# Kernel tuning notes

Measured on AMD Instinct MI355X. Metric: run time of the kernel, lower is better.

Reference implementation:

```python
import jax, jax.numpy as jnp
import numpy as np
from jax import lax

EPS = 2e-05


def _conv2d(x, w, b, stride):
    # x: [B,C,H,W], w: [O,I,3,3] (OIHW), VALID padding
    y = lax.conv_general_dilated(x, w, (stride, stride), 'VALID',
                                 dimension_numbers=('NCHW', 'OIHW', 'NCHW'))
    return y + b[None, :, None, None]


def _reflect_pad(x):
    return jnp.pad(x, ((0, 0), (0, 0), (1, 1), (1, 1)), mode='reflect')


def _transfer(cont_feat, styl_feat):
    # cont_feat, styl_feat: [B, N, H, W]
    B, N, H, W = cont_feat.shape
    xc = cont_feat.reshape(B, N, -1)   # [B,N,Mc]
    xs = styl_feat.reshape(B, N, -1)   # [B,N,Ms]
    I = jnp.eye(N, dtype=xc.dtype)

    # whitening of content
    mc = jnp.mean(xc, axis=-1, keepdims=True)
    xc0 = xc - mc
    cov_c = jnp.einsum('bnm,bkm->bnk', xc0, xc0) / (xc0.shape[-1] - 1)
    Lc = jnp.linalg.cholesky(cov_c + EPS * I)  # eps*I regularization (torch retry loop)
    inv_Lc = jnp.linalg.inv(Lc)
    whiten = jnp.einsum('bnk,bkm->bnm', inv_Lc, xc0)

    # coloring with style statistics
    ms = jnp.mean(xs, axis=-1, keepdims=True)
    xs0 = xs - ms
    cov_s = jnp.einsum('bnm,bkm->bnk', xs0, xs0) / (xs0.shape[-1] - 1)
    Ls = jnp.linalg.cholesky(cov_s + EPS * I)
    colored = jnp.einsum('bnk,bkm->bnm', Ls, whiten) + ms
    return colored.reshape(B, N, H, W)


def setup_inputs() -> dict:
    key = jax.random.key(0)
    k1, k2, k3, k4 = jax.random.split(key, 4)
    B, C, H, W = 8, 128, 256, 256
    cont_feat = jax.random.normal(k1, (B, C, H, W), dtype=jnp.float32)
    styl_feat = jax.random.normal(k2, (B, C, H, W), dtype=jnp.float32)
    # conv params (kaiming-ish scaling)
    fan1 = C * 9
    W1 = jax.random.normal(k3, (C, C, 3, 3), dtype=jnp.float32) / np.sqrt(fan1)
    b1 = jnp.zeros((C,), dtype=jnp.float32)
    W2 = jax.random.normal(k4, (2 * C, C, 3, 3), dtype=jnp.float32) / np.sqrt(fan1)
    b2 = jnp.zeros((2 * C,), dtype=jnp.float32)
    return {'cont_feat': cont_feat, 'styl_feat': styl_feat,
            'W1': W1, 'b1': b1, 'W2': W2, 'b2': b2}


def reference(cont_feat, styl_feat, W1, b1, W2, b2):
    cs = _transfer(cont_feat, styl_feat)          # [B,C,H,W]
    x = _conv2d(_reflect_pad(cs), W1, b1, 2)      # [B,C,H/2,W/2]
    x = jax.nn.relu(x)
    out = _conv2d(_reflect_pad(x), W2, b2, 1)     # [B,2C,H/2,W/2]
    return out
```

## Files before the change

### kernel.cpp

```cpp
#include <hip/hip_runtime.h>
#include <hip/hip_bf16.h>

#define B_  8
#define C_  128
#define M_  65536
#define EPSV 2e-05f

typedef __attribute__((ext_vector_type(8))) short bf16x8;
typedef __attribute__((ext_vector_type(4))) float f32x4;

#define MFMA(a, b, c) __builtin_amdgcn_mfma_f32_16x16x32_bf16((a), (b), (c), 0, 0, 0)

__device__ __forceinline__ short f2b(float f) {
    unsigned u = __float_as_uint(f);
    u = (u + 0x7FFFu + ((u >> 16) & 1u)) >> 16;
    return (short)u;
}

__device__ __forceinline__ int swz(int px, int c) {
    return px * 256 + ((((c >> 3) ^ (px & 15)) << 4) | ((c & 7) << 1));
}

__device__ __forceinline__ int rot(int i, int k) {
    return i * 128 + ((((k >> 2) + i) & 31) << 2) + (k & 3);
}

__global__ __launch_bounds__(256) void k_prep(const float* W1, const float* W2,
                                              short* wp1, short* wp2) {
    int idx = blockIdx.x * 256 + threadIdx.x;
    if (idx < 9 * 128 * 128) {
        int c = idx & 127, o = (idx >> 7) & 127, rs = idx >> 14;
        wp1[idx] = f2b(W1[(o * 128 + c) * 9 + rs]);
    }
    idx -= 9 * 128 * 128;
    if (idx >= 0 && idx < 9 * 256 * 128) {
        int c = idx & 127, o = (idx >> 7) & 255, rs = idx >> 15;
        wp2[idx] = f2b(W2[(o * 128 + c) * 9 + rs]);
    }
}

__global__ __launch_bounds__(256, 2) void k_gram(const float* cont, const float* styl,
                                                 float* part, float* S) {
    __shared__ short ls[128 * 136];
    __shared__ float ssum[128 * 32];
    int bx = blockIdx.x;
    int chunk = bx & 31, which = (bx >> 5) & 1, b = bx >> 6;
    const float* X = (which ? styl : cont) + (size_t)b * C_ * M_ + chunk * 2048;
    int tid = threadIdx.x, lane = tid & 63, wid = tid >> 6;
    int kg = tid & 31, r0 = tid >> 5;

    float sacc[16];
    #pragma unroll
    for (int p = 0; p < 16; ++p) sacc[p] = 0.f;
    f32x4 acc[2][8];
    for (int u = 0; u < 2; ++u)
        for (int j = 0; j < 8; ++j) acc[u][j] = (f32x4){0.f, 0.f, 0.f, 0.f};

    float4 pf[16];
    #pragma unroll
    for (int p = 0; p < 16; ++p)
        pf[p] = *(const float4*)(X + (size_t)(r0 + p * 8) * M_ + kg * 4);

    for (int it = 0; it < 16; ++it) {
        #pragma unroll
        for (int p = 0; p < 16; ++p) {
            int row = r0 + p * 8;
            float4 v = pf[p];
            sacc[p] += v.x + v.y + v.z + v.w;
            union { __hip_bfloat162 h[2]; unsigned long long u; } pk;
            pk.h[0] = __float22bfloat162_rn(make_float2(v.x, v.y));
            pk.h[1] = __float22bfloat162_rn(make_float2(v.z, v.w));
            *(unsigned long long*)(ls + row * 136 + kg * 4) = pk.u;
        }
        if (it < 15) {
            int kb = (it + 1) * 128;
            #pragma unroll
            for (int p = 0; p < 16; ++p)
                pf[p] = *(const float4*)(X + (size_t)(r0 + p * 8) * M_ + kb + kg * 4);
        }
        asm volatile("s_waitcnt lgkmcnt(0)" ::: "memory");
        __builtin_amdgcn_sched_barrier(0);
        __builtin_amdgcn_s_barrier();
        for (int ks = 0; ks < 4; ++ks) {
            int co = ks * 32 + (lane >> 4) * 8;
            bf16x8 a[2], bbf[8];
            for (int u = 0; u < 2; ++u) {
                int row = (wid * 2 + u) * 16 + (lane & 15);
                a[u] = *(const bf16x8*)(ls + row * 136 + co);
            }
            for (int j = 0; j < 8; ++j) {
                int row = j * 16 + (lane & 15);
                bbf[j] = *(const bf16x8*)(ls + row * 136 + co);
            }
            for (int u = 0; u < 2; ++u)
                for (int j = 0; j < 8; ++j)
                    acc[u][j] = MFMA(a[u], bbf[j], acc[u][j]);
        }
        __builtin_amdgcn_sched_barrier(0);
        __builtin_amdgcn_s_barrier();
    }
    __syncthreads();
    for (int p = 0; p < 16; ++p) ssum[(r0 + p * 8) * 32 + kg] = sacc[p];
    __syncthreads();
    float* Sp = S + ((size_t)which * 8 + b) * 128;
    if (tid < 128) {
        float s = 0.f;
        for (int q = 0; q < 32; ++q) s += ssum[tid * 32 + q];
        atomicAdd(&Sp[tid], s);
    }
    float* Pp = part + ((size_t)((which * 8 + b) * 32 + chunk)) * 16384;
    for (int u = 0; u < 2; ++u) {
        int rowb = (wid * 2 + u) * 16 + (lane >> 4) * 4;
        for (int j = 0; j < 8; ++j) {
            int col = j * 16 + (lane & 15);
            for (int e = 0; e < 4; ++e)
                Pp[(rowb + e) * 128 + col] = acc[u][j][e];
        }
    }
}

__global__ __launch_bounds__(256) void k_gsum(const float* part, float* G) {
    int idx = blockIdx.x * 256 + threadIdx.x;
    int m = idx >> 14, e = idx & 16383;
    const float* p = part + (size_t)m * 32 * 16384 + e;
    float s = 0.f;
    #pragma unroll
    for (int c = 0; c < 32; ++c) s += p[(size_t)c * 16384];
    G[idx] = s;
}

__global__ __launch_bounds__(128) void k_chol(const float* G, const float* S,
                                              float* LcT, float* Lsg) {
    __shared__ float A[128 * 128];
    int wb = blockIdx.x;
    int i = threadIdx.x;
    const float invM = 1.f / 65536.f;
    const float invM1 = 1.f / 65535.f;
    const float* Gp = G + (size_t)wb * 16384;
    const float* Sp = S + (size_t)wb * 128;
    float mui = Sp[i] * invM;

    for (int j = 0; j <= i; ++j) {
        float muj = Sp[j] * invM;
        float cv = (Gp[i * 128 + j] - 65536.f * mui * muj) * invM1;
        if (j == i) cv += EPSV;
        A[rot(i, j)] = cv;
    }
    __syncthreads();

    #pragma unroll
    for (int bb = 0; bb < 4; ++bb) {
        const int jb0 = bb * 32, bend = jb0 + 32;
        float t[32], u[32], t0[32];
        #pragma unroll
        for (int kk = 0; kk < 32; ++kk) t0[kk] = A[rot(i, jb0 + kk)];
        #pragma unroll
        for (int jj = 0; jj < 32; ++jj) {
            const int j = jb0 + jj;
            float dot = 0.f;
            #pragma unroll
            for (int kk = 0; kk < jj; ++kk)
                dot += u[kk] * A[rot(j, jb0 + kk)];
            float raw = t0[jj] - dot;
            if (i >= j) A[rot(i, j)] = raw;
            __syncthreads();
            float pr = A[rot(j, j)];
            float piv = sqrtf(pr);
            float rpj = 1.f / piv;
            float tv = (i > j) ? raw * rpj : (i == j ? piv : 0.f);
            t[jj] = tv;
            u[jj] = tv * rpj;
        }
        #pragma unroll
        for (int kk = 0; kk < 32; ++kk) {
            int j = jb0 + kk;
            if (i >= j) A[rot(i, j)] = t[kk];
        }
        __syncthreads();
        if (bb < 3) {
            if (i >= bend) {
                int jmax = (i & ~63) + 64;
                for (int j4 = bend; j4 < jmax; j4 += 4) {
                    float* rp_ = A + i * 128 + ((((j4 >> 2) + i) & 31) << 2);
                    float4 r = *(float4*)rp_;
                    #pragma unroll
                    for (int g = 0; g < 8; ++g) {
                        int kc = (jb0 >> 2) + g;
                        float4 c0 = *(const float4*)(A + (j4 + 0) * 128 + (((kc + j4 + 0) & 31) << 2));
                        float4 c1 = *(const float4*)(A + (j4 + 1) * 128 + (((kc + j4 + 1) & 31) << 2));
                        float4 c2 = *(const float4*)(A + (j4 + 2) * 128 + (((kc + j4 + 2) & 31) << 2));
                        float4 c3 = *(const float4*)(A + (j4 + 3) * 128 + (((kc + j4 + 3) & 31) << 2));
                        float ta = t[g * 4], tb = t[g * 4 + 1], tc = t[g * 4 + 2], td = t[g * 4 + 3];
                        r.x -= ta * c0.x + tb * c0.y + tc * c0.z + td * c0.w;
                        r.y -= ta * c1.x + tb * c1.y + tc * c1.z + td * c1.w;
                        r.z -= ta * c2.x + tb * c2.y + tc * c2.z + td * c2.w;
                        r.w -= ta * c3.x + tb * c3.y + tc * c3.z + td * c3.w;
                    }
                    *(float4*)rp_ = r;
                }
            }
            __syncthreads();
        }
    }
    __syncthreads();
    if (wb < 8) {
        float* dst = LcT + (size_t)wb * 16384;
        for (int j = 0; j <= i; ++j)
            dst[j * 128 + i] = A[rot(i, j)];
    } else {
        float4* dst = (float4*)(Lsg + (size_t)(wb - 8) * 16384);
        const float4* src = (const float4*)A;
        for (int t = i; t < 4096; t += 128) dst[t] = src[t];
    }
}

__global__ __launch_bounds__(128) void k_trsm(const float* LcT, const float* Lsg,
                                              const float* S, short* Tb, float* Vv) {
    __shared__ float A[128 * 128];
    int b = blockIdx.x;
    int i = threadIdx.x;
    const float invM = 1.f / 65536.f;
    const float* Lc = LcT + (size_t)b * 16384;
    {
        const float4* src = (const float4*)(Lsg + (size_t)b * 16384);
        float4* dst = (float4*)A;
        for (int t = i; t < 4096; t += 128) dst[t] = src[t];
    }
    __syncthreads();
    float lsdia = A[rot(i, i)];
    float rdia = 1.f / Lc[i * 128 + i];
    float tii = lsdia * rdia;
    __syncthreads();
    for (int j = 0; j < 127; ++j)
        if (i > j) A[rot(j, i)] = Lc[j * 128 + i];
    A[rot(i, i)] = rdia;
    __syncthreads();

    #pragma unroll
    for (int bb = 3; bb >= 0; --bb) {
        const int jb0 = bb * 32, bend = jb0 + 32;
        float t[32], ls0[32];
        #pragma unroll
        for (int kk = 0; kk < 32; ++kk) ls0[kk] = A[rot(i, jb0 + kk)];
        #pragma unroll
        for (int jj = 31; jj >= 0; --jj) {
            const int j = jb0 + jj;
            float dot = (i < bend) ? tii * A[rot(j, i)] : 0.f;
            #pragma unroll
            for (int kk = jj + 1; kk < 32; ++kk)
                dot += t[kk] * A[rot(j, jb0 + kk)];
            float val = (ls0[jj] - dot) * A[rot(j, j)];
            t[jj] = (j < i) ? val : 0.f;
        }
        #pragma unroll
        for (int kk = 0; kk < 32; ++kk) {
            int j = jb0 + kk;
            if (j < i) A[rot(i, j)] = t[kk];
            if (j == i) t[kk] = tii;
        }
        if (jb0 > 0 && i >= jb0) {
            for (int j4 = 0; j4 < jb0; j4 += 4) {
                float* rp = A + i * 128 + ((((j4 >> 2) + i) & 31) << 2);
                float4 r = *(float4*)rp;
                #pragma unroll
                for (int g = 0; g < 8; ++g) {
                    int kc = (jb0 >> 2) + g;
                    float4 c0 = *(const float4*)(A + (j4 + 0) * 128 + (((kc + j4 + 0) & 31) << 2));
                    float4 c1 = *(const float4*)(A + (j4 + 1) * 128 + (((kc + j4 + 1) & 31) << 2));
                    float4 c2 = *(const float4*)(A + (j4 + 2) * 128 + (((kc + j4 + 2) & 31) << 2));
                    float4 c3 = *(const float4*)(A + (j4 + 3) * 128 + (((kc + j4 + 3) & 31) << 2));
                    float ta = t[g * 4], tb2 = t[g * 4 + 1], tc = t[g * 4 + 2], td = t[g * 4 + 3];
                    r.x -= ta * c0.x + tb2 * c0.y + tc * c0.z + td * c0.w;
                    r.y -= ta * c1.x + tb2 * c1.y + tc * c1.z + td * c1.w;
                    r.z -= ta * c2.x + tb2 * c2.y + tc * c2.z + td * c2.w;
                    r.w -= ta * c3.x + tb2 * c3.y + tc * c3.z + td * c3.w;
                }
                *(float4*)rp = r;
            }
        }
    }
    const float* Sc = S + (size_t)b * 128;
    const float* Ss = S + (size_t)(8 + b) * 128;
    float vdot = 0.f;
    short* Tr = Tb + (size_t)b * 16384 + i * 128;
    for (int j = 0; j < 128; ++j) {
        float t = (j < i) ? A[rot(i, j)] : (j == i ? tii : 0.f);
        Tr[j] = f2b(t);
        if (j <= i) vdot += t * (Sc[j] * invM);
    }
    Vv[b * 128 + i] = Ss[i] * invM - vdot;
}

__global__ __launch_bounds__(256) void k_transform(const float* cont, const short* Tb,
                                                   const float* Vv, short* colored) {
    __shared__ short ls[16384];
    char* lsb = (char*)ls;
    int bx = blockIdx.x;
    int b = bx >> 9, p0 = (bx & 511) << 7;
    int tid = threadIdx.x, lane = tid & 63, wid = tid >> 6;

    {
        int px = tid & 127, ch = tid >> 7;
        const float* Xp = cont + (size_t)b * C_ * M_ + p0 + px;
        for (int it = 0; it < 16; ++it) {
            int c0 = it * 8 + ch * 4;
            float x0 = Xp[(size_t)(c0 + 0) * M_];
            float x1 = Xp[(size_t)(c0 + 1) * M_];
            float x2 = Xp[(size_t)(c0 + 2) * M_];
            float x3 = Xp[(size_t)(c0 + 3) * M_];
            union { short s[4]; unsigned long long u; } pk;
            pk.s[0] = f2b(x0); pk.s[1] = f2b(x1); pk.s[2] = f2b(x2); pk.s[3] = f2b(x3);
            *(unsigned long long*)(lsb + swz(px, c0)) = pk.u;
        }
    }
    __syncthreads();
    f32x4 acc[8][2];
    for (int pg = 0; pg < 8; ++pg)
        for (int u = 0; u < 2; ++u) acc[pg][u] = (f32x4){0.f, 0.f, 0.f, 0.f};
    const short* Tbase = Tb + (size_t)b * 16384;
    for (int kc = 0; kc < 4; ++kc) {
        int co = kc * 32 + (lane >> 4) * 8;
        bf16x8 bfr[2], afr[8];
        for (int u = 0; u < 2; ++u) {
            int chn = (wid * 2 + u) * 16 + (lane & 15);
            bfr[u] = *(const bf16x8*)(Tbase + chn * 128 + co);
        }
        for (int pg = 0; pg < 8; ++pg) {
            int px = pg * 16 + (lane & 15);
            afr[pg] = *(const bf16x8*)(lsb + swz(px, co));
        }
        for (int pg = 0; pg < 8; ++pg)
            for (int u = 0; u < 2; ++u)
                acc[pg][u] = MFMA(afr[pg], bfr[u], acc[pg][u]);
    }
    __syncthreads();
    for (int u = 0; u < 2; ++u) {
        int chn = (wid * 2 + u) * 16 + (lane & 15);
        float vv = Vv[b * 128 + chn];
        for (int pg = 0; pg < 8; ++pg)
            for (int e = 0; e < 4; ++e) {
                int px = pg * 16 + (lane >> 4) * 4 + e;
                *(short*)(lsb + swz(px, chn)) = f2b(acc[pg][u][e] + vv);
            }
    }
    __syncthreads();
    short* dst = colored + ((size_t)b * M_ + p0) * 128;
    for (int it = 0; it < 8; ++it) {
        int gid = tid + it * 256;
        int px = gid >> 4, gr = gid & 15;
        bf16x8 v = *(const bf16x8*)(lsb + px * 256 + ((gr ^ (px & 15)) << 4));
        *(bf16x8*)(dst + (size_t)px * 128 + gr * 8) = v;
    }
}

__global__ __launch_bounds__(256) void k_conv1(const short* colored, const short* wp1,
                                               const float* b1, short* out1) {
    __shared__ short ls[130 * 128];
    char* lsb = (char*)ls;
    int x0 = blockIdx.x * 64, y = blockIdx.y, b = blockIdx.z;
    int tid = threadIdx.x, lane = tid & 63, wid = tid >> 6;

    f32x4 acc[4][2];
    for (int pg = 0; pg < 4; ++pg)
        for (int u = 0; u < 2; ++u) acc[pg][u] = (f32x4){0.f, 0.f, 0.f, 0.f};

    for (int r = 0; r < 3; ++r) {
        int grow = 2 * y - 1 + r;
        if (grow < 0) grow = -grow;
        __syncthreads();
        const short* src = colored + ((size_t)b * M_ + grow * 256) * 128;
        for (int it = 0; it < 9; ++it) {
            int gid = tid + it * 256;
            if (gid < 130 * 16) {
                int L = gid >> 4, gr = gid & 15;
                int gcol = 2 * x0 - 1 + L;
                if (gcol < 0) gcol = -gcol;
                else if (gcol > 255) gcol = 510 - gcol;
                bf16x8 v = *(const bf16x8*)(src + (size_t)gcol * 128 + gr * 8);
                *(bf16x8*)(lsb + L * 256 + ((gr ^ (L & 15)) << 4)) = v;
            }
        }
        __syncthreads();
        for (int s = 0; s < 3; ++s)
            for (int kc = 0; kc < 4; ++kc) {
                int co = kc * 32 + (lane >> 4) * 8;
                bf16x8 afr[4], bfr[2];
                for (int pg = 0; pg < 4; ++pg) {
                    int L = (pg * 16 + (lane & 15)) * 2 + s;
                    afr[pg] = *(const bf16x8*)(lsb + swz(L, co));
                }
                const short* wb = wp1 + (r * 3 + s) * 128 * 128;
                for (int u = 0; u < 2; ++u) {
                    int o = (wid * 2 + u) * 16 + (lane & 15);
                    bfr[u] = *(const bf16x8*)(wb + o * 128 + co);
                }
                for (int pg = 0; pg < 4; ++pg)
                    for (int u = 0; u < 2; ++u)
                        acc[pg][u] = MFMA(afr[pg], bfr[u], acc[pg][u]);
            }
    }
    __syncthreads();
    for (int u = 0; u < 2; ++u) {
        int o = (wid * 2 + u) * 16 + (lane & 15);
        float bias = b1[o];
        for (int pg = 0; pg < 4; ++pg)
            for (int e = 0; e < 4; ++e) {
                int px = pg * 16 + (lane >> 4) * 4 + e;
                float v = acc[pg][u][e] + bias;
                v = v > 0.f ? v : 0.f;
                *(short*)(lsb + swz(px, o)) = f2b(v);
            }
    }
    __syncthreads();
    short* dst = out1 + ((size_t)b * 16384 + y * 128 + x0) * 128;
    for (int it = 0; it < 4; ++it) {
        int gid = tid + it * 256;
        int px = gid >> 4, gr = gid & 15;
        bf16x8 v = *(const bf16x8*)(lsb + px * 256 + ((gr ^ (px & 15)) << 4));
        *(bf16x8*)(dst + (size_t)px * 128 + gr * 8) = v;
    }
}

__global__ __launch_bounds__(256) void k_conv2(const short* out1, const short* wp2,
                                               const float* b2, float* outp) {
    __shared__ short ls[66 * 128];
    char* lsb = (char*)ls;
    int x0 = blockIdx.x * 64, y = blockIdx.y, b = blockIdx.z;
    int tid = threadIdx.x, lane = tid & 63, wid = tid >> 6;

    f32x4 acc[4][4];
    for (int pg = 0; pg < 4; ++pg)
        for (int u = 0; u < 4; ++u) acc[pg][u] = (f32x4){0.f, 0.f, 0.f, 0.f};

    for (int r = 0; r < 3; ++r) {
        int grow = y - 1 + r;
        if (grow < 0) grow = -grow;
        else if (grow > 127) grow = 254 - grow;
        __syncthreads();
        const short* src = out1 + ((size_t)b * 16384 + grow * 128) * 128;
        for (int it = 0; it < 5; ++it) {
            int gid = tid + it * 256;
            if (gid < 66 * 16) {
                int L = gid >> 4, gr = gid & 15;
                int gcol = x0 - 1 + L;
                if (gcol < 0) gcol = -gcol;
                else if (gcol > 127) gcol = 254 - gcol;
                bf16x8 v = *(const bf16x8*)(src + (size_t)gcol * 128 + gr * 8);
                *(bf16x8*)(lsb + L * 256 + ((gr ^ (L & 15)) << 4)) = v;
            }
        }
        __syncthreads();
        for (int s = 0; s < 3; ++s)
            for (int kc = 0; kc < 4; ++kc) {
                int co = kc * 32 + (lane >> 4) * 8;
                bf16x8 afr[4], bfr[4];
                for (int pg = 0; pg < 4; ++pg) {
                    int L = pg * 16 + (lane & 15) + s;
                    afr[pg] = *(const bf16x8*)(lsb + swz(L, co));
                }
                const short* wb = wp2 + (r * 3 + s) * 256 * 128;
                for (int u = 0; u < 4; ++u) {
                    int o = (wid * 4 + u) * 16 + (lane & 15);
                    bfr[u] = *(const bf16x8*)(wb + o * 128 + co);
                }
                for (int pg = 0; pg < 4; ++pg)
                    for (int u = 0; u < 4; ++u)
                        acc[pg][u] = MFMA(afr[pg], bfr[u], acc[pg][u]);
            }
    }
    for (int u = 0; u < 4; ++u) {
        int o = (wid * 4 + u) * 16 + (lane & 15);
        float bias = b2[o];
        float* dst = outp + ((size_t)b * 256 + o) * 16384 + y * 128 + x0;
        for (int pg = 0; pg < 4; ++pg) {
            float4 v;
            v.x = acc[pg][u][0] + bias;
            v.y = acc[pg][u][1] + bias;
            v.z = acc[pg][u][2] + bias;
            v.w = acc[pg][u][3] + bias;
            *(float4*)(dst + pg * 16 + (lane >> 4) * 4) = v;
        }
    }
}

extern "C" void kernel_launch(void* const* d_in, const int* in_sizes, int n_in,
                              void* d_out, int out_size, void* d_ws, size_t ws_size,
                              hipStream_t stream) {
    const float* cont = (const float*)d_in[0];
    const float* styl = (const float*)d_in[1];
    const float* W1 = (const float*)d_in[2];
    const float* b1 = (const float*)d_in[3];
    const float* W2 = (const float*)d_in[4];
    const float* b2 = (const float*)d_in[5];
    float* outp = (float*)d_out;
    char* ws = (char*)d_ws;

    float* G       = (float*)(ws + 0x0);
    float* S       = (float*)(ws + 0x100000);
    float* LcT     = (float*)(ws + 0x110000);
    float* Lsg     = (float*)(ws + 0x190000);
    short* Tb      = (short*)(ws + 0x210000);
    float* Vv      = (float*)(ws + 0x250000);
    short* wp1     = (short*)(ws + 0x260000);
    short* wp2     = (short*)(ws + 0x2A8000);
    short* colored = (short*)(ws + 0x400000);
    float* part    = (float*)(ws + 0x400000);
    short* out1    = (short*)(ws + 0x8400000);

    hipMemsetAsync(S, 0, 0x2000, stream);
    k_prep<<<1728, 256, 0, stream>>>(W1, W2, wp1, wp2);
    k_gram<<<512, 256, 0, stream>>>(cont, styl, part, S);
    k_gsum<<<1024, 256, 0, stream>>>(part, G);
    k_chol<<<16, 128, 0, stream>>>(G, S, LcT, Lsg);
    k_trsm<<<8, 128, 0, stream>>>(LcT, Lsg, S, Tb, Vv);
    k_transform<<<4096, 256, 0, stream>>>(cont, Tb, Vv, colored);
    k_conv1<<<dim3(2, 128, 8), 256, 0, stream>>>(colored, wp1, b1, out1);
    k_conv2<<<dim3(2, 128, 8), 256, 0, stream>>>(out1, wp2, b2, outp);
}
```

Before: 755.3 us.

## Fuse Cholesky and triangular solve into one kernel keeping factors in LDS

Merges the separate Cholesky and TRSM kernels into a single kernel where each block factors both content and style covariances concurrently (two 128-thread halves) and then computes Ls*inv(Lc) directly from shared memory. This removes the global round trip of the factors, one kernel launch, and the transposed strided load of Lc. Covariance construction and panel loads now use float4 accesses, and the bf16 output is packed. The block uses 128KB of LDS, and only half the threads do work in the serial solve phase.

```diff
diff --git a/kernel.cpp b/kernel.cpp
--- a/kernel.cpp
+++ b/kernel.cpp
@@ -129,42 +129,75 @@
     G[idx] = s;
 }
 
-__global__ __launch_bounds__(128) void k_chol(const float* G, const float* S,
-                                              float* LcT, float* Lsg) {
-    __shared__ float A[128 * 128];
-    int wb = blockIdx.x;
-    int i = threadIdx.x;
+__global__ __launch_bounds__(256) void k_solve(const float* G, const float* S,
+                                               short* Tb, float* Vv) {
+    __shared__ float A[16384];
+    __shared__ float Bm[16384];
+    __shared__ float muA[128], muB[128];
+    int b = blockIdx.x;
+    int tid = threadIdx.x;
+    int half = tid >> 7, i = tid & 127;
     const float invM = 1.f / 65536.f;
     const float invM1 = 1.f / 65535.f;
-    const float* Gp = G + (size_t)wb * 16384;
-    const float* Sp = S + (size_t)wb * 128;
-    float mui = Sp[i] * invM;
-
-    for (int j = 0; j <= i; ++j) {
-        float muj = Sp[j] * invM;
-        float cv = (Gp[i * 128 + j] - 65536.f * mui * muj) * invM1;
-        if (j == i) cv += EPSV;
-        A[rot(i, j)] = cv;
-    }
-    __syncthreads();
-
-    #pragma unroll
+    float* M = half ? Bm : A;
+    float* mu = half ? muB : muA;
+    const float* Gp = G + ((size_t)(half * 8 + b)) * 16384;
+    const float* Sp = S + ((size_t)(half * 8 + b)) * 128;
+
+    mu[i] = Sp[i] * invM;
+    __syncthreads();
+
+    {
+        const float4* G4 = (const float4*)Gp;
+        int c4 = i & 31;
+        #pragma unroll 4
+        for (int bt = 0; bt < 4; ++bt) {
+            float4 gv[8];
+            #pragma unroll
+            for (int q = 0; q < 8; ++q) gv[q] = G4[i + 128 * (bt * 8 + q)];
+            #pragma unroll
+            for (int q = 0; q < 8; ++q) {
+                int it = bt * 8 + q;
+                int r = (i >> 5) + 4 * it;
+                float mur = mu[r] * 65536.f;
+                float4 mc = *(const float4*)&mu[c4 * 4];
+                float4 g = gv[q], cv;
+                cv.x = (g.x - mur * mc.x) * invM1;
+                cv.y = (g.y - mur * mc.y) * invM1;
+                cv.z = (g.z - mur * mc.z) * invM1;
+                cv.w = (g.w - mur * mc.w) * invM1;
+                int c0 = c4 * 4;
+                if (r == c0 + 0) cv.x += EPSV;
+                if (r == c0 + 1) cv.y += EPSV;
+                if (r == c0 + 2) cv.z += EPSV;
+                if (r == c0 + 3) cv.w += EPSV;
+                *(float4*)(M + r * 128 + (((c4 + r) & 31) << 2)) = cv;
+            }
+        }
+    }
+    __syncthreads();
+
+    #pragma unroll 1
     for (int bb = 0; bb < 4; ++bb) {
         const int jb0 = bb * 32, bend = jb0 + 32;
         float t[32], u[32], t0[32];
         #pragma unroll
-        for (int kk = 0; kk < 32; ++kk) t0[kk] = A[rot(i, jb0 + kk)];
+        for (int g = 0; g < 8; ++g) {
+            float4 v = *(const float4*)(M + i * 128 + ((((jb0 >> 2) + g + i) & 31) << 2));
+            t0[g * 4 + 0] = v.x; t0[g * 4 + 1] = v.y;
+            t0[g * 4 + 2] = v.z; t0[g * 4 + 3] = v.w;
+        }
         #pragma unroll
         for (int jj = 0; jj < 32; ++jj) {
             const int j = jb0 + jj;
             float dot = 0.f;
             #pragma unroll
             for (int kk = 0; kk < jj; ++kk)
-                dot += u[kk] * A[rot(j, jb0 + kk)];
+                dot += u[kk] * M[rot(j, jb0 + kk)];
             float raw = t0[jj] - dot;
-            if (i >= j) A[rot(i, j)] = raw;
+            if (i >= j) M[rot(i, j)] = raw;
             __syncthreads();
-            float pr = A[rot(j, j)];
+            float pr = M[rot(j, j)];
             float piv = sqrtf(pr);
             float rpj = 1.f / piv;
             float tv = (i > j) ? raw * rpj : (i == j ? piv : 0.f);
@@ -172,24 +205,26 @@
             u[jj] = tv * rpj;
         }
         #pragma unroll
-        for (int kk = 0; kk < 32; ++kk) {
-            int j = jb0 + kk;
-            if (i >= j) A[rot(i, j)] = t[kk];
+        for (int g = 0; g < 8; ++g) {
+            float4 v = {t[g * 4], t[g * 4 + 1], t[g * 4 + 2], t[g * 4 + 3]};
+            if (i >= bend - 1 || 1) {  }
+            *(float4*)(M + i * 128 + ((((jb0 >> 2) + g + i) & 31) << 2)) =
+                (i >= jb0) ? v : *(float4*)(M + i * 128 + ((((jb0 >> 2) + g + i) & 31) << 2));
         }
         __syncthreads();
         if (bb < 3) {
             if (i >= bend) {
                 int jmax = (i & ~63) + 64;
                 for (int j4 = bend; j4 < jmax; j4 += 4) {
-                    float* rp_ = A + i * 128 + ((((j4 >> 2) + i) & 31) << 2);
+                    float* rp_ = M + i * 128 + ((((j4 >> 2) + i) & 31) << 2);
                     float4 r = *(float4*)rp_;
                     #pragma unroll
                     for (int g = 0; g < 8; ++g) {
                         int kc = (jb0 >> 2) + g;
-                        float4 c0 = *(const float4*)(A + (j4 + 0) * 128 + (((kc + j4 + 0) & 31) << 2));
-                        float4 c1 = *(const float4*)(A + (j4 + 1) * 128 + (((kc + j4 + 1) & 31) << 2));
-                        float4 c2 = *(const float4*)(A + (j4 + 2) * 128 + (((kc + j4 + 2) & 31) << 2));
-                        float4 c3 = *(const float4*)(A + (j4 + 3) * 128 + (((kc + j4 + 3) & 31) << 2));
+                        float4 c0 = *(const float4*)(M + (j4 + 0) * 128 + (((kc + j4 + 0) & 31) << 2));
+                        float4 c1 = *(const float4*)(M + (j4 + 1) * 128 + (((kc + j4 + 1) & 31) << 2));
+                        float4 c2 = *(const float4*)(M + (j4 + 2) * 128 + (((kc + j4 + 2) & 31) << 2));
+                        float4 c3 = *(const float4*)(M + (j4 + 3) * 128 + (((kc + j4 + 3) & 31) << 2));
                         float ta = t[g * 4], tb = t[g * 4 + 1], tc = t[g * 4 + 2], td = t[g * 4 + 3];
                         r.x -= ta * c0.x + tb * c0.y + tc * c0.z + td * c0.w;
                         r.y -= ta * c1.x + tb * c1.y + tc * c1.z + td * c1.w;
@@ -203,92 +238,89 @@
         }
     }
     __syncthreads();
-    if (wb < 8) {
-        float* dst = LcT + (size_t)wb * 16384;
-        for (int j = 0; j <= i; ++j)
-            dst[j * 128 + i] = A[rot(i, j)];
-    } else {
-        float4* dst = (float4*)(Lsg + (size_t)(wb - 8) * 16384);
-        const float4* src = (const float4*)A;
-        for (int t = i; t < 4096; t += 128) dst[t] = src[t];
-    }
-}
-
-__global__ __launch_bounds__(128) void k_trsm(const float* LcT, const float* Lsg,
-                                              const float* S, short* Tb, float* Vv) {
-    __shared__ float A[128 * 128];
-    int b = blockIdx.x;
-    int i = threadIdx.x;
-    const float invM = 1.f / 65536.f;
-    const float* Lc = LcT + (size_t)b * 16384;
-    {
-        const float4* src = (const float4*)(Lsg + (size_t)b * 16384);
-        float4* dst = (float4*)A;
-        for (int t = i; t < 4096; t += 128) dst[t] = src[t];
-    }
-    __syncthreads();
-    float lsdia = A[rot(i, i)];
-    float rdia = 1.f / Lc[i * 128 + i];
-    float tii = lsdia * rdia;
-    __syncthreads();
-    for (int j = 0; j < 127; ++j)
-        if (i > j) A[rot(j, i)] = Lc[j * 128 + i];
-    A[rot(i, i)] = rdia;
-    __syncthreads();
-
-    #pragma unroll
-    for (int bb = 3; bb >= 0; --bb) {
-        const int jb0 = bb * 32, bend = jb0 + 32;
-        float t[32], ls0[32];
-        #pragma unroll
-        for (int kk = 0; kk < 32; ++kk) ls0[kk] = A[rot(i, jb0 + kk)];
-        #pragma unroll
-        for (int jj = 31; jj >= 0; --jj) {
-            const int j = jb0 + jj;
-            float dot = (i < bend) ? tii * A[rot(j, i)] : 0.f;
-            #pragma unroll
-            for (int kk = jj + 1; kk < 32; ++kk)
-                dot += t[kk] * A[rot(j, jb0 + kk)];
-            float val = (ls0[jj] - dot) * A[rot(j, j)];
-            t[jj] = (j < i) ? val : 0.f;
-        }
-        #pragma unroll
-        for (int kk = 0; kk < 32; ++kk) {
-            int j = jb0 + kk;
-            if (j < i) A[rot(i, j)] = t[kk];
-            if (j == i) t[kk] = tii;
-        }
-        if (jb0 > 0 && i >= jb0) {
-            for (int j4 = 0; j4 < jb0; j4 += 4) {
-                float* rp = A + i * 128 + ((((j4 >> 2) + i) & 31) << 2);
-                float4 r = *(float4*)rp;
+
+    float rdia = 0.f, tii = 0.f;
+    if (half == 0) {
+        rdia = 1.f / A[rot(i, i)];
+        tii = Bm[rot(i, i)] * rdia;
+    }
+    __syncthreads();
+    if (half == 0) {
+        A[rot(i, i)] = rdia;
+        Bm[rot(i, i)] = tii;
+    }
+    __syncthreads();
+
+    #pragma unroll 1
+    for (int b2 = 3; b2 >= 0; --b2) {
+        const int jb0 = b2 * 32, bend = jb0 + 32;
+        if (half == 0) {
+            float t[32], l0[32];
+            #pragma unroll
+            for (int g = 0; g < 8; ++g) {
+                float4 v = *(const float4*)(Bm + i * 128 + ((((jb0 >> 2) + g + i) & 31) << 2));
+                l0[g * 4 + 0] = v.x; l0[g * 4 + 1] = v.y;
+                l0[g * 4 + 2] = v.z; l0[g * 4 + 3] = v.w;
+            }
+            #pragma unroll
+            for (int jj = 31; jj >= 0; --jj) {
+                const int j = jb0 + jj;
+                float dot = (i < bend) ? tii * A[rot(i, j)] : 0.f;
+                #pragma unroll
+                for (int kk = jj + 1; kk < 32; ++kk) {
+                    const int k = jb0 + kk;
+                    dot += t[kk] * A[rot(k, j)];
+                }
+                float val = (l0[jj] - dot) * A[rot(j, j)];
+                t[jj] = (j < i) ? val : (j == i ? tii : 0.f);
+            }
+            #pragma unroll
+            for (int g = 0; g < 8; ++g) {
+                float4 v = {t[g * 4], t[g * 4 + 1], t[g * 4 + 2], t[g * 4 + 3]};
+                *(float4*)(Bm + i * 128 + ((((jb0 >> 2) + g + i) & 31) << 2)) = v;
+            }
+        }
+        __syncthreads();
+        if (jb0 > 0) {
+            if (i >= jb0) {
+                float th[32];
                 #pragma unroll
                 for (int g = 0; g < 8; ++g) {
-                    int kc = (jb0 >> 2) + g;
-                    float4 c0 = *(const float4*)(A + (j4 + 0) * 128 + (((kc + j4 + 0) & 31) << 2));
-                    float4 c1 = *(const float4*)(A + (j4 + 1) * 128 + (((kc + j4 + 1) & 31) << 2));
-                    float4 c2 = *(const float4*)(A + (j4 + 2) * 128 + (((kc + j4 + 2) & 31) << 2));
-                    float4 c3 = *(const float4*)(A + (j4 + 3) * 128 + (((kc + j4 + 3) & 31) << 2));
-                    float ta = t[g * 4], tb2 = t[g * 4 + 1], tc = t[g * 4 + 2], td = t[g * 4 + 3];
-                    r.x -= ta * c0.x + tb2 * c0.y + tc * c0.z + td * c0.w;
-                    r.y -= ta * c1.x + tb2 * c1.y + tc * c1.z + td * c1.w;
-                    r.z -= ta * c2.x + tb2 * c2.y + tc * c2.z + td * c2.w;
-                    r.w -= ta * c3.x + tb2 * c3.y + tc * c3.z + td * c3.w;
-                }
-                *(float4*)rp = r;
-            }
-        }
-    }
-    const float* Sc = S + (size_t)b * 128;
-    const float* Ss = S + (size_t)(8 + b) * 128;
-    float vdot = 0.f;
-    short* Tr = Tb + (size_t)b * 16384 + i * 128;
-    for (int j = 0; j < 128; ++j) {
-        float t = (j < i) ? A[rot(i, j)] : (j == i ? tii : 0.f);
-        Tr[j] = f2b(t);
-        if (j <= i) vdot += t * (Sc[j] * invM);
-    }
-    Vv[b * 128 + i] = Ss[i] * invM - vdot;
+                    float4 v = *(const float4*)(Bm + i * 128 + ((((jb0 >> 2) + g + i) & 31) << 2));
+                    th[g * 4 + 0] = v.x; th[g * 4 + 1] = v.y;
+                    th[g * 4 + 2] = v.z; th[g * 4 + 3] = v.w;
+                }
+                for (int j4 = half * 4; j4 < jb0; j4 += 8) {
+                    float* rp = Bm + i * 128 + ((((j4 >> 2) + i) & 31) << 2);
+                    float4 r = *(float4*)rp;
+                    #pragma unroll
+                    for (int kk = 0; kk < 32; ++kk) {
+                        const int k = jb0 + kk;
+                        float4 lc = *(const float4*)(A + k * 128 + ((((j4 >> 2) + k) & 31) << 2));
+                        r.x -= th[kk] * lc.x; r.y -= th[kk] * lc.y;
+                        r.z -= th[kk] * lc.z; r.w -= th[kk] * lc.w;
+                    }
+                    *(float4*)rp = r;
+                }
+            }
+            __syncthreads();
+        }
+    }
+
+    if (half == 0) {
+        float vdot = 0.f;
+        short* Tr = Tb + (size_t)b * 16384 + i * 128;
+        for (int j4 = 0; j4 < 32; ++j4) {
+            float4 tv = *(const float4*)(Bm + i * 128 + (((j4 + i) & 31) << 2));
+            float4 mc = *(const float4*)&muA[j4 * 4];
+            vdot += tv.x * mc.x + tv.y * mc.y + tv.z * mc.z + tv.w * mc.w;
+            union { __hip_bfloat162 h[2]; unsigned long long u; } pk;
+            pk.h[0] = __float22bfloat162_rn(make_float2(tv.x, tv.y));
+            pk.h[1] = __float22bfloat162_rn(make_float2(tv.z, tv.w));
+            *(unsigned long long*)(Tr + j4 * 4) = pk.u;
+        }
+        Vv[b * 128 + i] = muB[i] - vdot;
+    }
 }
 
 __global__ __launch_bounds__(256) void k_transform(const float* cont, const short* Tb,
@@ -497,12 +529,10 @@
 
     float* G       = (float*)(ws + 0x0);
     float* S       = (float*)(ws + 0x100000);
-    float* LcT     = (float*)(ws + 0x110000);
-    float* Lsg     = (float*)(ws + 0x190000);
-    short* Tb      = (short*)(ws + 0x210000);
-    float* Vv      = (float*)(ws + 0x250000);
-    short* wp1     = (short*)(ws + 0x260000);
-    short* wp2     = (short*)(ws + 0x2A8000);
+    short* Tb      = (short*)(ws + 0x110000);
+    float* Vv      = (float*)(ws + 0x150000);
+    short* wp1     = (short*)(ws + 0x160000);
+    short* wp2     = (short*)(ws + 0x1A8000);
     short* colored = (short*)(ws + 0x400000);
     float* part    = (float*)(ws + 0x400000);
     short* out1    = (short*)(ws + 0x8400000);
@@ -511,8 +541,7 @@
     k_prep<<<1728, 256, 0, stream>>>(W1, W2, wp1, wp2);
     k_gram<<<512, 256, 0, stream>>>(cont, styl, part, S);
     k_gsum<<<1024, 256, 0, stream>>>(part, G);
-    k_chol<<<16, 128, 0, stream>>>(G, S, LcT, Lsg);
-    k_trsm<<<8, 128, 0, stream>>>(LcT, Lsg, S, Tb, Vv);
+    k_solve<<<8, 256, 0, stream>>>(G, S, Tb, Vv);
     k_transform<<<4096, 256, 0, stream>>>(cont, Tb, Vv, colored);
     k_conv1<<<dim3(2, 128, 8), 256, 0, stream>>>(colored, wp1, b1, out1);
     k_conv2<<<dim3(2, 128, 8), 256, 0, stream>>>(out1, wp2, b2, outp);
```

After: 641.3 us. 15.1% less time.
